# Optimization experiments

Hardware: AMD Instinct MI355X
Metric: run time of the kernel (lower is better)

The kernel has to match this reference:

```python
import jax, jax.numpy as jnp
import numpy as np

B, C, H, W = 2, 64, 128, 128
HEADS, DH = 8, 32
DN = ('NCHW', 'OIHW', 'NCHW')


def _conv(x, w, pad):
    return jax.lax.conv_general_dilated(x, w, (1, 1), [(pad, pad), (pad, pad)], dimension_numbers=DN)


def _rconv3(x, w):
    # Conv3x3 module: ReflectionPad2d(1) then 3x3 VALID conv, no bias
    xp = jnp.pad(x, ((0, 0), (0, 0), (1, 1), (1, 1)), mode='reflect')
    return jax.lax.conv_general_dilated(xp, w, (1, 1), 'VALID', dimension_numbers=DN)


def _prelu(x, a):
    return jnp.where(x > 0, x, a * x)


def _l2n(x):
    # F.normalize(p=2, dim=-1), eps=1e-12
    return x / jnp.maximum(jnp.linalg.norm(x, axis=-1, keepdims=True), 1e-12)


def _ln(y, g, b):
    mu = y.mean(-1, keepdims=True)
    v = ((y - mu) ** 2).mean(-1, keepdims=True)
    return (y - mu) / jnp.sqrt(v + 1e-5) * g + b


def _qco(x, w1, sw, sb, t1w, t1b, t2w, t2b):
    # QCO_C with level_num == C
    b, Cc = x.shape[0], x.shape[1]
    L = Cc
    x1 = _rconv3(x, w1)
    x_ave = _conv(jnp.mean(x1, (2, 3), keepdims=True), sw, 0) + sb[None, :, None, None]  # [b,C,1,1]
    xq = x_ave.reshape(b, Cc)
    mn = xq.min(-1, keepdims=True)
    mx = xq.max(-1, keepdims=True)
    qs = jnp.arange(L, dtype=x.dtype)
    ql = (2.0 * qs + 1.0) / (2.0 * L) * (mx - mn) + mn  # [b,L]
    inter = (ql[:, 1] - ql[:, 0])[:, None, None]  # [b,1,1]
    quant = 1.0 - jnp.abs(ql[:, None, :] - xq[:, :, None])  # [b,C,L]
    quant = quant * (quant > 1.0 - inter)
    sta = quant.sum(1)  # [b,L]
    sta = sta / sta.sum(-1, keepdims=True)
    out = jnp.concatenate([sta[:, :, None, None], x_ave], axis=1)  # [b,2C,1,1]
    out = jax.nn.relu(_conv(out, t1w, 0) + t1b[None, :, None, None])
    out = jax.nn.relu(_conv(out, t2w, 0) + t2b[None, :, None, None])
    return out  # [b,C,1,1]


def _attention(x, w_down, w_mid, w_up, wq_l, wk_m, wv_m, wq_h, rescale,
               w_proj_l, b_proj_l, w_proj_h, b_proj_h,
               qco_w1, qco_sca_w, qco_sca_b, qco_t1_w, qco_t1_b, qco_t2_w, qco_t2_b,
               rsp_w1, rsp_prelu, rsp_w2, c31_w1, c31_prelu, c31_w2, c31_w3):
    b, Cc, Hh, Ww = x.shape
    n = Hh * Ww
    # QKV conv projections (Conv2d, zero pad 1, no bias)
    xCL = jnp.moveaxis(_conv(x, w_down, 1), 1, -1)  # [b,h,w,C]
    xCM = jnp.moveaxis(_conv(x, w_mid, 1), 1, -1)   # [b,h,w,2C]
    xCH = jnp.moveaxis(_conv(x, w_up, 1), 1, -1)    # [b,h,w,3C]
    xL = xCL.reshape(b, n, Cc)
    xM = xCM.reshape(b, n, 2 * Cc)
    xH = xCH.reshape(b, n, 3 * Cc)

    def to_heads(t, d):  # [b,n,heads*d] -> [b,heads,d,n]
        return t.reshape(b, n, HEADS, d).transpose(0, 2, 3, 1)

    q_l = _l2n(to_heads(xL @ wq_l.T, DH))            # [b,heads,DH,n]
    k_m = _l2n(to_heads(xM @ wk_m.T, 2 * DH))        # [b,heads,2DH,n]
    v_m = to_heads(xM @ wv_m.T, 2 * DH)              # [b,heads,2DH,n]
    q_h = _l2n(to_heads(xH @ wq_h.T, 3 * DH))        # [b,heads,3DH,n]

    attn_l = jax.nn.softmax(jnp.einsum('bhdn,bhen->bhde', q_l, k_m) * rescale, axis=-1)  # [b,heads,DH,2DH]
    attn_h = jax.nn.softmax(jnp.einsum('bhdn,bhen->bhde', q_h, k_m) * rescale, axis=-1)  # [b,heads,3DH,2DH]

    x_l = jnp.einsum('bhde,bhen->bhdn', attn_l, v_m).transpose(0, 3, 1, 2).reshape(b, n, HEADS * DH)
    x_h = jnp.einsum('bhde,bhen->bhdn', attn_h, v_m).transpose(0, 3, 1, 2).reshape(b, n, HEADS * 3 * DH)
    # NOTE: torch code does .view(b, c, h, w) on [b, n, c] output -> raw memory reinterpretation,
    # which is exactly jnp.reshape here (faithful to the original, including this quirk).
    out_cl = (x_l @ w_proj_l.T + b_proj_l).reshape(b, Cc, Hh, Ww)
    out_ch = (x_h @ w_proj_h.T + b_proj_h).reshape(b, 3 * Cc, Hh, Ww)

    Hcat = jnp.concatenate([out_cl, out_ch], axis=1)  # [b,4C,h,w]
    H_out = _rconv3(_prelu(_rconv3(Hcat, rsp_w1), rsp_prelu), rsp_w2)  # ReshapeBlock -> [b,C,h,w]
    att_before = _qco(jnp.moveaxis(xCL, -1, 1), qco_w1, qco_sca_w, qco_sca_b,
                      qco_t1_w, qco_t1_b, qco_t2_w, qco_t2_b)  # [b,C,1,1]
    t = _prelu(_rconv3(H_out, c31_w1), c31_prelu)
    H_add = _conv(_rconv3(t, c31_w2), c31_w3, 0)  # Conv3_1
    return H_add + H_out * att_before


def _ff_block(z, g, bb, w1, b1, w2, b2):
    # PreNorm(LayerNorm over channel) + FeedForward(Linear, LeakyReLU(0.01), Linear)
    y = jnp.moveaxis(z, 1, -1)
    y = _ln(y, g, bb)
    y = y @ w1.T + b1
    y = jnp.where(y > 0, y, 0.01 * y)
    y = y @ w2.T + b2
    return jnp.moveaxis(y, -1, 1)


def _forward(x, w_down, w_mid, w_up, wq_l, wk_m, wv_m, wq_h, rescale,
             w_proj_l, b_proj_l, w_proj_h, b_proj_h,
             qco_w1, qco_sca_w, qco_sca_b, qco_t1_w, qco_t1_b, qco_t2_w, qco_t2_b,
             rsp_w1, rsp_prelu, rsp_w2, c31_w1, c31_prelu, c31_w2, c31_w3,
             ln1_g, ln1_b, ff1_w1, ff1_b1, ff1_w2, ff1_b2,
             ln2_g, ln2_b, ff2_w1, ff2_b1, ff2_w2, ff2_b2):
    out1 = _attention(x, w_down, w_mid, w_up, wq_l, wk_m, wv_m, wq_h, rescale,
                      w_proj_l, b_proj_l, w_proj_h, b_proj_h,
                      qco_w1, qco_sca_w, qco_sca_b, qco_t1_w, qco_t1_b, qco_t2_w, qco_t2_b,
                      rsp_w1, rsp_prelu, rsp_w2, c31_w1, c31_prelu, c31_w2, c31_w3) + x
    out2 = _ff_block(out1, ln1_g, ln1_b, ff1_w1, ff1_b1, ff1_w2, ff1_b2) + out1
    out3 = _ff_block(out2, ln2_g, ln2_b, ff2_w1, ff2_b1, ff2_w2, ff2_b2) + out1
    return out3


def setup_inputs() -> dict:
    keys = iter(jax.random.split(jax.random.key(0), 48))

    def rn(shape, s=0.05):
        return (jax.random.normal(next(keys), shape, jnp.float32) * s)

    d = {
        'x': rn((B, C, H, W), 1.0),
        'w_down': rn((C, C, 3, 3)), 'w_mid': rn((2 * C, C, 3, 3)), 'w_up': rn((3 * C, C, 3, 3)),
        'wq_l': rn((HEADS * DH, C)), 'wk_m': rn((2 * HEADS * DH, 2 * C)),
        'wv_m': rn((2 * HEADS * DH, 2 * C)), 'wq_h': rn((3 * HEADS * DH, 3 * C)),
        'rescale': jnp.ones((HEADS, 1, 1), jnp.float32),
        'w_proj_l': rn((C, HEADS * DH)), 'b_proj_l': rn((C,)),
        'w_proj_h': rn((3 * C, 3 * HEADS * DH)), 'b_proj_h': rn((3 * C,)),
        'qco_w1': rn((C, C, 3, 3)), 'qco_sca_w': rn((C, C, 1, 1)), 'qco_sca_b': rn((C,)),
        'qco_t1_w': rn((C, 2 * C, 1, 1)), 'qco_t1_b': rn((C,)),
        'qco_t2_w': rn((C, C, 1, 1)), 'qco_t2_b': rn((C,)),
        'rsp_w1': rn((C, 4 * C, 3, 3)), 'rsp_prelu': jnp.array(0.25, jnp.float32), 'rsp_w2': rn((C, C, 3, 3)),
        'c31_w1': rn((C, C, 3, 3)), 'c31_prelu': jnp.array(0.25, jnp.float32),
        'c31_w2': rn((C, C, 3, 3)), 'c31_w3': rn((C, C, 1, 1)),
        'ln1_g': jnp.ones((C,), jnp.float32), 'ln1_b': jnp.zeros((C,), jnp.float32),
        'ff1_w1': rn((C, C)), 'ff1_b1': rn((C,)), 'ff1_w2': rn((C, C)), 'ff1_b2': rn((C,)),
        'ln2_g': jnp.ones((C,), jnp.float32), 'ln2_b': jnp.zeros((C,), jnp.float32),
        'ff2_w1': rn((C, C)), 'ff2_b1': rn((C,)), 'ff2_w2': rn((C, C)), 'ff2_b2': rn((C,)),
    }
    return d


def reference(x, w_down, w_mid, w_up, wq_l, wk_m, wv_m, wq_h, rescale,
              w_proj_l, b_proj_l, w_proj_h, b_proj_h,
              qco_w1, qco_sca_w, qco_sca_b, qco_t1_w, qco_t1_b, qco_t2_w, qco_t2_b,
              rsp_w1, rsp_prelu, rsp_w2, c31_w1, c31_prelu, c31_w2, c31_w3,
              ln1_g, ln1_b, ff1_w1, ff1_b1, ff1_w2, ff1_b2,
              ln2_g, ln2_b, ff2_w1, ff2_b1, ff2_w2, ff2_b2):
    return _forward(x, w_down, w_mid, w_up, wq_l, wk_m, wv_m, wq_h, rescale,
                    w_proj_l, b_proj_l, w_proj_h, b_proj_h,
                    qco_w1, qco_sca_w, qco_sca_b, qco_t1_w, qco_t1_b, qco_t2_w, qco_t2_b,
                    rsp_w1, rsp_prelu, rsp_w2, c31_w1, c31_prelu, c31_w2, c31_w3,
                    ln1_g, ln1_b, ff1_w1, ff1_b1, ff1_w2, ff1_b2,
                    ln2_g, ln2_b, ff2_w1, ff2_b1, ff2_w2, ff2_b2)
```

## Files before the change

kernel.cpp:

```cpp
#include <hip/hip_runtime.h>
#include <hip/hip_bf16.h>
#include <stdint.h>

typedef __hip_bfloat16 bf16;
typedef __attribute__((ext_vector_type(8))) __bf16 bf8v;
typedef __attribute__((ext_vector_type(8))) short short8;
typedef __attribute__((ext_vector_type(4))) short short4v;
typedef __attribute__((ext_vector_type(4))) float f32x4;
#define DEVINL __device__ __forceinline__
#define MFMA16(a,b,c) __builtin_amdgcn_mfma_f32_16x16x32_bf16((a),(b),(c),0,0,0)

DEVINL short f2bs(float f) { bf16 h = __float2bfloat16(f); return *reinterpret_cast<short*>(&h); }
DEVINL float bs2f(short s) { bf16 h = *reinterpret_cast<bf16*>(&s); return __bfloat162float(h); }


static const size_t OFF_ZBF   = 0;
static const size_t OFF_WTQ   = 29360128;
static const size_t OFF_WTR1  = 29802496;
static const size_t OFF_WTR2  = 30097408;
static const size_t OFF_WTC1  = 30171136;
static const size_t OFF_WTF   = 30244864;
static const size_t OFF_W1T   = 30318592;
static const size_t OFF_SCAWT = 30466048;
static const size_t OFF_T1WT  = 30482432;
static const size_t OFF_T2WT  = 30515200;
static const size_t OFF_GB    = 31645696;
static const size_t OFF_WQLB  = 32235520;
static const size_t OFF_WKMB  = 32268288;
static const size_t OFF_WQHB  = 32399360;
static const size_t OFF_T1    = 41082880;
static const size_t OFF_UL    = 41345024;
static const size_t OFF_UK    = 41476096;
static const size_t OFF_T1H   = 42000384;
static const size_t OFF_UH    = 42786816;
static const size_t OFF_NORMS = 43966464;
static const size_t OFF_ATTL  = 43978752;
static const size_t OFF_ATTH  = 44109824;
static const size_t OFF_WEL   = 44503040;
static const size_t OFF_WEH   = 44765184;
static const size_t OFF_ACATB = 45813760;
static const size_t OFF_TSUM  = 45944832;
static const size_t OFF_ATTB  = 45949440;
static const size_t OFF_HCATB = 45949952;
static const size_t OFF_MIDB  = 62727168;
static const size_t OFF_HOUTB = 66921472;
static const size_t OFF_OUT1  = 71115776;
static const size_t OFF_GPART = 79504384;
static const size_t OFF_HCATT = 79504384;
static const size_t OFF_XT    = 98378752;
static const size_t WS_BYTES  = 102573056;

__global__ __launch_bounds__(256) void k_transp(const float* __restrict__ x,
                                                short* __restrict__ xt) {
  __shared__ short sT[64][72];
  const int t = threadIdx.x, b = blockIdx.z, p0 = blockIdx.x * 64;
  for (int i = t; i < 1024; i += 256) {
    int c = i >> 4, p4 = (i & 15) * 4;
    float4 g = *(const float4*)&x[(((size_t)(b * 64 + c)) << 14) + p0 + p4];
    sT[p4 + 0][c] = f2bs(g.x);
    sT[p4 + 1][c] = f2bs(g.y);
    sT[p4 + 2][c] = f2bs(g.z);
    sT[p4 + 3][c] = f2bs(g.w);
  }
  __syncthreads();
  for (int i = t; i < 512; i += 256) {
    int p = i >> 3, co = (i & 7) * 8;
    *(short8*)&xt[((((size_t)b << 14) + p0 + p)) * 64 + co] = *(short8*)&sT[p][co];
  }
}

__global__ __launch_bounds__(256) void k_transph(const short* __restrict__ hc,
                                                 short* __restrict__ ht) {
  __shared__ short sT[64][72];
  const int t = threadIdx.x, b = blockIdx.z, p0 = blockIdx.x * 64, c0 = blockIdx.y * 64;
  for (int i = t; i < 512; i += 256) {
    int c = i >> 3, qo = (i & 7) * 8;
    short8 v = *(const short8*)&hc[(((size_t)(b * 256 + c0 + c)) << 14) + p0 + qo];
#pragma unroll
    for (int u = 0; u < 8; u++) sT[qo + u][c] = v[u];
  }
  __syncthreads();
  for (int i = t; i < 512; i += 256) {
    int q = i >> 3, co = (i & 7) * 8;
    *(short8*)&ht[((size_t)(b * 16384 + p0 + q)) * 256 + c0 + co] = *(short8*)&sT[q][co];
  }
}

__global__ void k_prep_all(const float* __restrict__ wd, const float* __restrict__ wm,
                           const float* __restrict__ wu, const float* __restrict__ rw1,
                           const float* __restrict__ rw2, const float* __restrict__ cw1,
                           const float* __restrict__ wql, const float* __restrict__ wkm,
                           const float* __restrict__ wqh,
                           const float* __restrict__ c31w3, const float* __restrict__ c31w2,
                           const float* __restrict__ qw1, const float* __restrict__ qscaw,
                           const float* __restrict__ qt1w, const float* __restrict__ qt2w,
                           bf16* __restrict__ wtq, bf16* __restrict__ wtr1,
                           bf16* __restrict__ wtr2, bf16* __restrict__ wtc1,
                           bf16* __restrict__ wqlb, bf16* __restrict__ wkmb,
                           bf16* __restrict__ wqhb, bf16* __restrict__ wtf,
                           float* __restrict__ w1t, float* __restrict__ scawt,
                           float* __restrict__ t1wt, float* __restrict__ t2wt) {
  int i = blockIdx.x * 256 + threadIdx.x;
  if (i < 221184) {
    int tap = i / 24576, r = i % 24576, oc = r >> 6, ic = r & 63;
    float v;
    if (oc < 64)       v = wd[(oc * 64 + ic) * 9 + tap];
    else if (oc < 192) v = wm[((oc - 64) * 64 + ic) * 9 + tap];
    else               v = wu[((oc - 192) * 64 + ic) * 9 + tap];
    wtq[i] = __float2bfloat16(v);
  } else if (i < 368640) {
    int j = i - 221184;
    int tap = j / 16384, r = j % 16384, oc = r >> 8, ic = r & 255;
    wtr1[j] = __float2bfloat16(rw1[(oc * 256 + ic) * 9 + tap]);
  } else if (i < 405504) {
    int j = i - 368640;
    int tap = j / 4096, r = j % 4096, oc = r >> 6, ic = r & 63;
    wtr2[j] = __float2bfloat16(rw2[(oc * 64 + ic) * 9 + tap]);
  } else if (i < 442368) {
    int j = i - 405504;
    int tap = j / 4096, r = j % 4096, oc = r >> 6, ic = r & 63;
    wtc1[j] = __float2bfloat16(cw1[(oc * 64 + ic) * 9 + tap]);
  } else if (i < 458752) {
    int j = i - 442368; wqlb[j] = __float2bfloat16(wql[j]);
  } else if (i < 524288) {
    int j = i - 458752; wkmb[j] = __float2bfloat16(wkm[j]);
  } else if (i < 671744) {
    int j = i - 524288; wqhb[j] = __float2bfloat16(wqh[j]);
  } else if (i < 708608) {
    int j = i - 671744;
    int tap = j / 4096, r = j % 4096, o = r >> 6, ic = r & 63;
    float s = 0.f;
    for (int m = 0; m < 64; m++)
      s = fmaf(c31w3[o * 64 + m], c31w2[(m * 64 + ic) * 9 + tap], s);
    wtf[j] = __float2bfloat16(s);
  } else if (i < 745472) {
    int o = i - 708608;
    int c = o & 63, rest = o >> 6, jj = rest / 9, tap = rest % 9;
    w1t[o] = qw1[(c * 64 + jj) * 9 + tap];
  } else if (i < 749568) {
    int o = i - 745472;
    int c = o & 63, jj = o >> 6;
    scawt[o] = qscaw[c * 64 + jj];
  } else if (i < 757760) {
    int o = i - 749568;
    int c = o & 63, jj = o >> 6;
    t1wt[o] = qt1w[c * 128 + jj];
  } else if (i < 761856) {
    int o = i - 757760;
    int c = o & 63, jj = o >> 6;
    t2wt[o] = qt2w[c * 64 + jj];
  }
}

__global__ __launch_bounds__(256) void k_convq(
    const short* __restrict__ xt, const short* __restrict__ wtq,
    bf16* __restrict__ zbf)
{
  __shared__ short sX[3][130][72];
  const int t = threadIdx.x, lane = t & 63, wv = t >> 6;
  const int y = blockIdx.x, ocg = blockIdx.y, b = blockIdx.z;

  for (int i = t; i < 3120; i += 256) {
    int col = i % 130, rr = i / 130, row = rr % 3, ko = rr / 3;
    int gy = y + row - 1, gx = col - 1;
    short8 vv;
    if ((gy >= 0) & (gy < 128) & (gx >= 0) & (gx < 128)) {
      vv = *(const short8*)&xt[((size_t)b * 1048576 + (size_t)((gy << 7) + gx) * 64) + ko * 8];
    } else {
#pragma unroll
      for (int u = 0; u < 8; u++) vv[u] = 0;
    }
    *(short8*)&sX[row][col][ko * 8] = vv;
  }
  __syncthreads();

  const f32x4 zero = {0.f, 0.f, 0.f, 0.f};
  f32x4 acc[3][8];
#pragma unroll
  for (int m = 0; m < 3; m++)
#pragma unroll
    for (int n = 0; n < 8; n++) acc[m][n] = zero;

#pragma unroll
  for (int tap = 0; tap < 9; tap++) {
    const int ky = tap / 3, kx = tap % 3;
#pragma unroll
    for (int kk = 0; kk < 2; kk++) {
      const int kb = kk * 32 + (lane >> 4) * 8;
      bf8v a0 = *(const bf8v*)&wtq[(size_t)((tap * 384 + ocg * 192 + wv * 48 + (lane & 15)) * 64) + kb];
      bf8v a1 = *(const bf8v*)&wtq[(size_t)((tap * 384 + ocg * 192 + wv * 48 + 16 + (lane & 15)) * 64) + kb];
      bf8v a2 = *(const bf8v*)&wtq[(size_t)((tap * 384 + ocg * 192 + wv * 48 + 32 + (lane & 15)) * 64) + kb];
#pragma unroll
      for (int n = 0; n < 8; n++) {
        bf8v bfr = *(const bf8v*)&sX[ky][n * 16 + (lane & 15) + kx][kb];
        acc[0][n] = MFMA16(a0, bfr, acc[0][n]);
        acc[1][n] = MFMA16(a1, bfr, acc[1][n]);
        acc[2][n] = MFMA16(a2, bfr, acc[2][n]);
      }
    }
  }
#pragma unroll
  for (int m = 0; m < 3; m++) {
    const int oc0 = ocg * 192 + wv * 48 + m * 16 + ((lane >> 4) << 2);
#pragma unroll
    for (int n = 0; n < 8; n++) {
      const int px = n * 16 + (lane & 15);
#pragma unroll
      for (int r = 0; r < 4; r++)
        zbf[(((size_t)(b * 384 + oc0 + r)) << 14) + (y << 7) + px] = __float2bfloat16(acc[m][n][r]);
    }
  }
}

template<int EPI>
__global__ __launch_bounds__(256) void k_conv64(
    const short* __restrict__ in, int str, long bstride, int Cin,
    const short* __restrict__ Wt,
    short* __restrict__ outb, float* __restrict__ outf,
    const float* __restrict__ prelu_a,
    const short* __restrict__ houtpm, const float* __restrict__ attb,
    const float* __restrict__ x_nchw)
{
  __shared__ short sX[3][66][72];
  const int t = threadIdx.x, lane = t & 63, wv = t >> 6;
  const int y = blockIdx.x, x0 = blockIdx.y * 64, b = blockIdx.z;

  const f32x4 zero = {0.f, 0.f, 0.f, 0.f};
  f32x4 acc[4] = {zero, zero, zero, zero};

  for (int icb = 0; icb < Cin; icb += 64) {
    __syncthreads();
    for (int i = t; i < 1584; i += 256) {
      int col = i % 66, rr = i / 66, row = rr % 3, ko = rr / 3;
      int gy = y + row - 1, gx = x0 + col - 1;
      gy = gy < 0 ? 1 : (gy > 127 ? 126 : gy);
      gx = gx < 0 ? 1 : (gx > 127 ? 126 : gx);
      *(short8*)&sX[row][col][ko * 8] =
          *(const short8*)&in[(size_t)b * bstride + (size_t)((gy << 7) + gx) * str + icb + ko * 8];
    }
    __syncthreads();
#pragma unroll
    for (int tap = 0; tap < 9; tap++) {
      const int ky = tap / 3, kx = tap % 3;
#pragma unroll
      for (int kk = 0; kk < 2; kk++) {
        const int kb = kk * 32 + (lane >> 4) * 8;
        bf8v afr = *(const bf8v*)&Wt[(size_t)(tap * 64 + wv * 16 + (lane & 15)) * Cin + icb + kb];
#pragma unroll
        for (int n = 0; n < 4; n++) {
          bf8v bfr = *(const bf8v*)&sX[ky][n * 16 + (lane & 15) + kx][kb];
          acc[n] = MFMA16(afr, bfr, acc[n]);
        }
      }
    }
  }
  const int oc0 = wv * 16 + ((lane >> 4) << 2);
  const float aP = (EPI == 1) ? prelu_a[0] : 0.f;
#pragma unroll
  for (int n = 0; n < 4; n++) {
    const int gpx = (y << 7) + x0 + n * 16 + (lane & 15);
    if (EPI == 2) {
      short4v hv = *(const short4v*)&houtpm[((size_t)(b * 16384 + gpx)) * 64 + oc0];
      float4 av = *(const float4*)&attb[b * 64 + oc0];
      float4 o;
#pragma unroll
      for (int r = 0; r < 4; r++)
        (&o.x)[r] = acc[n][r] + bs2f(hv[r]) * (&av.x)[r] +
                    x_nchw[(((size_t)(b * 64 + oc0 + r)) << 14) + gpx];
      *(float4*)&outf[((size_t)(b * 16384 + gpx)) * 64 + oc0] = o;
    } else {
      short4v ss;
#pragma unroll
      for (int r = 0; r < 4; r++) {
        float v = acc[n][r];
        if (EPI == 1) v = v > 0.f ? v : aP * v;
        ss[r] = f2bs(v);
      }
      *(short4v*)&outb[((size_t)(b * 16384 + gpx)) * 64 + oc0] = ss;
    }
  }
}

__global__ __launch_bounds__(256) void k_gramm(const short* __restrict__ Z,
                                               float* __restrict__ Gp) {
  int rem = blockIdx.x, ti = 0;
  while (rem >= 6 - ti) { rem -= 6 - ti; ti++; }
  const int tj = ti + rem;
  const int kc = blockIdx.y, b = blockIdx.z;
  __shared__ short sA[64][72];
  __shared__ short sB[64][72];
  const int t = threadIdx.x, lane = t & 63, wv = t >> 6;
  const int wo = wv & 1, wp = wv >> 1;
  const f32x4 zero = {0.f, 0.f, 0.f, 0.f};
  f32x4 acc[2][2];
#pragma unroll
  for (int m = 0; m < 2; m++)
#pragma unroll
    for (int n = 0; n < 2; n++) acc[m][n] = zero;
  const size_t zb = (size_t)b * 6291456;
  const int k0 = kc * 1024;
  for (int ks = 0; ks < 1024; ks += 64) {
    __syncthreads();
    for (int i = t; i < 512; i += 256) {
      int r = i >> 3, ko = i & 7;
      *(short8*)&sA[r][ko * 8] =
          *(const short8*)&Z[zb + ((size_t)(ti * 64 + r) << 14) + k0 + ks + ko * 8];
      *(short8*)&sB[r][ko * 8] =
          *(const short8*)&Z[zb + ((size_t)(tj * 64 + r) << 14) + k0 + ks + ko * 8];
    }
    __syncthreads();
#pragma unroll
    for (int kk = 0; kk < 2; kk++) {
      const int kb = kk * 32 + (lane >> 4) * 8;
// ... 135 lines not shown
};

__global__ __launch_bounds__(256) void k_sgemm2b(Jobs2 J, bf16* __restrict__ Cb) {
  __shared__ float sa[16][17];
  __shared__ float sb[16][17];
  const int bx = blockIdx.x, z = blockIdx.y;
  int j = (bx >= J.b0[1]) ? 1 : 0;
  const int local = bx - J.b0[j];
  const int x = local % J.nx[j], y = local / J.nx[j];
  const int tx = threadIdx.x & 15, ty = threadIdx.x >> 4;
  const float* Ap = J.A[j];
  const float* Bp = J.B[j] + (size_t)z * J.sB[j];
  const int K = J.K[j], lda = J.lda[j];
  const int m = y * 16 + ty, n = x * 16 + tx;
  float acc = 0.f;
  for (int k0 = 0; k0 < K; k0 += 16) {
    sa[ty][tx] = Ap[(size_t)m * lda + k0 + tx];
    sb[ty][tx] = Bp[(size_t)(k0 + ty) * 128 + n];
    __syncthreads();
#pragma unroll
    for (int kk = 0; kk < 16; kk++) acc = fmaf(sa[ty][kk], sb[kk][tx], acc);
    __syncthreads();
  }
  Cb[(size_t)z * 32768 + J.co[j] + (size_t)m * 128 + n] = __float2bfloat16(acc);
}

__global__ __launch_bounds__(256) void k_norms2(
    const float* __restrict__ UL, const float* __restrict__ UK,
    const float* __restrict__ UH,
    const float* __restrict__ wql, const float* __restrict__ wkm,
    const float* __restrict__ wqh, float* __restrict__ norms) {
  const int t = threadIdx.x, lane = t & 63;
  const int row = blockIdx.x * 4 + (t >> 6);
  const int b = row >> 11 ? 1 : (row >= 1536 ? 1 : 0);
  const int r = row - b * 1536;
  const float* u; const float* wv; int K;
  if (r < 256)      { K = 64;  u = UL + (size_t)(b * 256 + r) * 64;          wv = wql + (size_t)r * 64; }
  else if (r < 768) { int e = r - 256; K = 128; u = UK + (size_t)(b * 512 + e) * 128; wv = wkm + (size_t)e * 128; }
  else              { int d = r - 768; K = 192; u = UH + (size_t)(b * 768 + d) * 192; wv = wqh + (size_t)d * 192; }
  float s = 0.f;
  for (int k = lane; k < K; k += 64) s = fmaf(u[k], wv[k], s);
#pragma unroll
  for (int o = 32; o; o >>= 1) s += __shfl_xor(s, o);
  if (lane == 0) norms[b * 1536 + r] = fmaxf(sqrtf(fmaxf(s, 0.f)), 1e-12f);
}

__global__ __launch_bounds__(256) void k_attn(
    const float* __restrict__ T1, const float* __restrict__ T1H,
    const float* __restrict__ wkm, const float* __restrict__ norms,
    const float* __restrict__ rescale,
    float* __restrict__ attL, float* __restrict__ attH)
{
  const int h = blockIdx.x, cy = blockIdx.y, b = blockIdx.z;
  const int t = threadIdx.x;
  __shared__ float sK[64 * 129];
  __shared__ float sQ[32 * 129];
  __shared__ float sNk[64];
  const int isL = (cy == 0);
  const int rbase = isL ? 0 : (cy - 1) * 32;
  const float* TQ = isL ? (T1 + (size_t)(b * 256 + h * 32) * 128)
                        : (T1H + (size_t)(b * 768 + h * 96 + rbase) * 128);
  for (int idx = t; idx < 8192; idx += 256) {
    int e = idx >> 7, k = idx & 127;
    sK[e * 129 + k] = wkm[(size_t)(h * 64 + e) * 128 + k];
  }
  for (int idx = t; idx < 4096; idx += 256) {
    int r = idx >> 7, k = idx & 127;
// ... 132 lines not shown
  sm[c] = acc * (1.f / 16384.f);
  __syncthreads();
  float xa = scab[c];
  for (int j = 0; j < 64; j++) xa = fmaf(scawt[(j << 6) + c], sm[j], xa);
  sxq[c] = xa;
  __syncthreads();
  float mn = xa, mx = xa;
#pragma unroll
  for (int o = 32; o; o >>= 1) {
    mn = fminf(mn, __shfl_xor(mn, o));
    mx = fmaxf(mx, __shfl_xor(mx, o));
  }
  float inter = (mx - mn) * (1.f / 64.f);
  float ql = (2.f * c + 1.f) / 128.f * (mx - mn) + mn;
  float sta = 0.f;
  for (int j = 0; j < 64; j++) {
    float q = 1.f - fabsf(ql - sxq[j]);
    sta += (q > 1.f - inter) ? q : 0.f;
  }
  float tot = sta;
#pragma unroll
  for (int o = 32; o; o >>= 1) tot += __shfl_xor(tot, o);
  sta = sta / fmaxf(tot, 1e-30f);
  scat[c] = sta; scat[64 + c] = xa;
  __syncthreads();
  float h = t1b[c];
  for (int j = 0; j < 128; j++) h = fmaf(t1wt[(j << 6) + c], scat[j], h);
  h = fmaxf(h, 0.f);
  sh1[c] = h;
  __syncthreads();
  float o2 = t2b[c];
  for (int j = 0; j < 64; j++) o2 = fmaf(t2wt[(j << 6) + c], sh1[j], o2);
  attb[b * 64 + c] = fmaxf(o2, 0.f);
}

__global__ __launch_bounds__(256) void k_ffm2(const float* __restrict__ out1pm,
    const float* g1, const float* be1, const float* w11, const float* b11,
    const float* w12, const float* b12,
    const float* g2, const float* be2, const float* w21, const float* b21,
    const float* w22, const float* b22,
    float* __restrict__ outp)
{
  __shared__ short sW4[4][64][72];
  __shared__ short sy[128][72];
  __shared__ float spar[8][64];

  const int t = threadIdx.x, lane = t & 63, wv = t >> 6;
  const int gp0 = blockIdx.x * 128;
  const int b = gp0 >> 14, p0 = gp0 & 16383;
  const int chq = ((lane >> 4) << 2);

  for (int idx = t; idx < 4096; idx += 256) {
    int oc = idx >> 6, k = idx & 63;
    sW4[0][oc][k] = f2bs(w11[idx]);
    sW4[1][oc][k] = f2bs(w12[idx]);
    sW4[2][oc][k] = f2bs(w21[idx]);
    sW4[3][oc][k] = f2bs(w22[idx]);
  }
  if (t < 64) {
    spar[0][t] = g1[t]; spar[1][t] = be1[t]; spar[2][t] = b11[t]; spar[3][t] = b12[t];
    spar[4][t] = g2[t]; spar[5][t] = be2[t]; spar[6][t] = b21[t]; spar[7][t] = b22[t];
  }
  float4 vv[4][2];
#pragma unroll
  for (int m = 0; m < 4; m++)
#pragma unroll
    for (int n = 0; n < 2; n++) {
      const int px = p0 + wv * 32 + n * 16 + (lane & 15);
      vv[m][n] = *(const float4*)&out1pm[((size_t)(b * 16384 + px)) * 64 + m * 16 + chq];
    }
  __syncthreads();

  const f32x4 zero = {0.f, 0.f, 0.f, 0.f};
  f32x4 acc[4][2];

#define LN_REG(SRCV, GI, BI)                                                     \
  {                                                                              \
    _Pragma("unroll")                                                            \
    for (int n = 0; n < 2; n++) {                                                \
      float s1 = 0.f, s2 = 0.f;                                                  \
      _Pragma("unroll")                                                          \
      for (int m = 0; m < 4; m++)                                                \
        _Pragma("unroll")                                                        \
        for (int r = 0; r < 4; r++) {                                            \
          float vx = (&SRCV[m][n].x)[r];                                         \
          s1 += vx; s2 += vx * vx;                                               \
        }                                                                        \
      s1 += __shfl_xor(s1, 16); s1 += __shfl_xor(s1, 32);                        \
      s2 += __shfl_xor(s2, 16); s2 += __shfl_xor(s2, 32);                        \
      float mu = s1 * (1.f / 64.f);                                              \
      float var = fmaxf(s2 * (1.f / 64.f) - mu * mu, 0.f);                       \
      float rstd = 1.f / sqrtf(var + 1e-5f);                                     \
      const int pxl = wv * 32 + n * 16 + (lane & 15);                            \
      _Pragma("unroll")                                                          \
      for (int m = 0; m < 4; m++) {                                              \
        short4v ss;                                                              \
        _Pragma("unroll")                                                        \
        for (int r = 0; r < 4; r++) {                                            \
          int ch = m * 16 + chq + r;                                             \
          ss[r] = f2bs(((&SRCV[m][n].x)[r] - mu) * rstd * spar[GI][ch] + spar[BI][ch]); \
        }                                                                        \
        *(short4v*)&sy[pxl][m * 16 + chq] = ss;                                  \
      }                                                                          \
    }                                                                            \
  }

#define MM_STAGE(SIDX)                                                           \
  {                                                                              \
    _Pragma("unroll")                                                            \
    for (int m = 0; m < 4; m++) { acc[m][0] = zero; acc[m][1] = zero; }          \
    _Pragma("unroll")                                                            \
    for (int kk = 0; kk < 2; kk++) {                                             \
      const int kb = kk * 32 + (lane >> 4) * 8;                                  \
      bf8v bfr0 = *(const bf8v*)&sy[wv * 32 + (lane & 15)][kb];                  \
      bf8v bfr1 = *(const bf8v*)&sy[wv * 32 + 16 + (lane & 15)][kb];             \
      _Pragma("unroll")                                                          \
      for (int m = 0; m < 4; m++) {                                              \
        bf8v afr = *(const bf8v*)&sW4[SIDX][m * 16 + (lane & 15)][kb];           \
        acc[m][0] = MFMA16(afr, bfr0, acc[m][0]);                                \
        acc[m][1] = MFMA16(afr, bfr1, acc[m][1]);                                \
      }                                                                          \
    }                                                                            \
  }

  LN_REG(vv, 0, 1);
  __syncthreads();
  MM_STAGE(0);
#pragma unroll
  for (int m = 0; m < 4; m++) {
#pragma unroll
    for (int n = 0; n < 2; n++) {
      const int pxl = wv * 32 + n * 16 + (lane & 15);
      short4v ss;
#pragma unroll
      for (int r = 0; r < 4; r++) {
        float h = acc[m][n][r] + spar[2][m * 16 + chq + r];
        h = h > 0.f ? h : 0.01f * h;
        ss[r] = f2bs(h);
      }
      *(short4v*)&sy[pxl][m * 16 + chq] = ss;
    }
  }
  __syncthreads();
  MM_STAGE(1);
  float4 o2v[4][2];
#pragma unroll
  for (int m = 0; m < 4; m++)
#pragma unroll
    for (int n = 0; n < 2; n++)
#pragma unroll
      for (int r = 0; r < 4; r++)
        (&o2v[m][n].x)[r] = acc[m][n][r] + spar[3][m * 16 + chq + r] + (&vv[m][n].x)[r];
  LN_REG(o2v, 4, 5);
  __syncthreads();
  MM_STAGE(2);
#pragma unroll
  for (int m = 0; m < 4; m++) {
#pragma unroll
    for (int n = 0; n < 2; n++) {
      const int pxl = wv * 32 + n * 16 + (lane & 15);
      short4v ss;
#pragma unroll
      for (int r = 0; r < 4; r++) {
        float h = acc[m][n][r] + spar[6][m * 16 + chq + r];
        h = h > 0.f ? h : 0.01f * h;
        ss[r] = f2bs(h);
      }
      *(short4v*)&sy[pxl][m * 16 + chq] = ss;
    }
  }
  __syncthreads();
  MM_STAGE(3);
#pragma unroll
  for (int m = 0; m < 4; m++)
#pragma unroll
    for (int n = 0; n < 2; n++) {
      const int pxl = wv * 32 + n * 16 + (lane & 15);
#pragma unroll
      for (int r = 0; r < 4; r++) {
        const int ch = m * 16 + chq + r;
        outp[(((size_t)(b * 64 + ch)) << 14) + p0 + pxl] =
            acc[m][n][r] + spar[7][ch] + (&vv[m][n].x)[r];
      }
    }
#undef LN_REG
#undef MM_STAGE
}

extern "C" void kernel_launch(void* const* d_in, const int* in_sizes, int n_in,
                              void* d_out, int out_size, void* d_ws, size_t ws_size,
                              hipStream_t stream)
{
  if (ws_size < WS_BYTES) return;
  char* ws = (char*)d_ws;

  const float* x       = (const float*)d_in[0];
  const float* w_down  = (const float*)d_in[1];
  const float* w_mid   = (const float*)d_in[2];
  const float* w_up    = (const float*)d_in[3];
  const float* wq_l    = (const float*)d_in[4];
  const float* wk_m    = (const float*)d_in[5];
  const float* wv_m    = (const float*)d_in[6];
  const float* wq_h    = (const float*)d_in[7];
  const float* rescale = (const float*)d_in[8];
  const float* w_proj_l= (const float*)d_in[9];
  const float* b_proj_l= (const float*)d_in[10];
  const float* w_proj_h= (const float*)d_in[11];
  const float* b_proj_h= (const float*)d_in[12];
  const float* qco_w1  = (const float*)d_in[13];
  const float* qsca_w  = (const float*)d_in[14];
  const float* qsca_b  = (const float*)d_in[15];
  const float* qt1_w   = (const float*)d_in[16];
  const float* qt1_b   = (const float*)d_in[17];
  const float* qt2_w   = (const float*)d_in[18];
  const float* qt2_b   = (const float*)d_in[19];
  const float* rsp_w1  = (const float*)d_in[20];
  const float* rsp_pr  = (const float*)d_in[21];
  const float* rsp_w2  = (const float*)d_in[22];
  const float* c31_w1  = (const float*)d_in[23];
// ... 15 lines not shown

  bf16*  zbf   = (bf16*)(ws + OFF_ZBF);
  bf16*  wtq   = (bf16*)(ws + OFF_WTQ);
  bf16*  wtr1  = (bf16*)(ws + OFF_WTR1);
  bf16*  wtr2  = (bf16*)(ws + OFF_WTR2);
  bf16*  wtc1  = (bf16*)(ws + OFF_WTC1);
  bf16*  wtf   = (bf16*)(ws + OFF_WTF);
  float* w1t   = (float*)(ws + OFF_W1T);
  float* scawt = (float*)(ws + OFF_SCAWT);
  float* t1wt  = (float*)(ws + OFF_T1WT);
  float* t2wt  = (float*)(ws + OFF_T2WT);
  bf16*  Gb    = (bf16*)(ws + OFF_GB);
  bf16*  wqlb  = (bf16*)(ws + OFF_WQLB);
  bf16*  wkmb  = (bf16*)(ws + OFF_WKMB);
  bf16*  wqhb  = (bf16*)(ws + OFF_WQHB);
  float* gpart = (float*)(ws + OFF_GPART);
  float* T1    = (float*)(ws + OFF_T1);
  float* UL    = (float*)(ws + OFF_UL);
  float* UK    = (float*)(ws + OFF_UK);
  float* T1H   = (float*)(ws + OFF_T1H);
  float* UH    = (float*)(ws + OFF_UH);
  float* norms = (float*)(ws + OFF_NORMS);
  float* attL  = (float*)(ws + OFF_ATTL);
  float* attH  = (float*)(ws + OFF_ATTH);
  float* WeL   = (float*)(ws + OFF_WEL);
  float* WeH   = (float*)(ws + OFF_WEH);
  bf16*  acatb = (bf16*)(ws + OFF_ACATB);
  float* tsum  = (float*)(ws + OFF_TSUM);
  float* attb  = (float*)(ws + OFF_ATTB);
  bf16*  hcatb = (bf16*)(ws + OFF_HCATB);
  short* hcatT = (short*)(ws + OFF_HCATT);
  short* midb  = (short*)(ws + OFF_MIDB);
  short* houtb = (short*)(ws + OFF_HOUTB);
  float* out1  = (float*)(ws + OFF_OUT1);
  short* xt    = (short*)(ws + OFF_XT);

  k_transp<<<dim3(256, 1, 2), 256, 0, stream>>>(x, xt);
  k_prep_all<<<dim3(2976), 256, 0, stream>>>(
      w_down, w_mid, w_up, rsp_w1, rsp_w2, c31_w1, wq_l, wk_m, wq_h,
      c31_w3, c31_w2, qco_w1, qsca_w, qt1_w, qt2_w,
      wtq, wtr1, wtr2, wtc1, wqlb, wkmb, wqhb, wtf,
      w1t, scawt, t1wt, t2wt);

  k_convq<<<dim3(128, 2, 2), 256, 0, stream>>>(xt, (const short*)wtq, zbf);

  k_gramm<<<dim3(21, 16, 2), 256, 0, stream>>>((const short*)zbf, gpart);
  k_gredb<<<dim3(1152), 256, 0, stream>>>(gpart, Gb);

  k_tsum2<<<dim3(128), 256, 0, stream>>>(zbf, tsum);

  MJobs5 M5;
  M5.A[0] = (const short*)wqlb; M5.lda[0] = 64;  M5.K[0] = 64;  M5.r0[0] = 0;   M5.c0[0] = 64;  M5.C[0] = T1;  M5.ldc[0] = 128; M5.sC[0] = 32768;  M5.nx[0] = 2;
  M5.A[1] = (const short*)wqlb; M5.lda[1] = 64;  M5.K[1] = 64;  M5.r0[1] = 0;   M5.c0[1] = 0;   M5.C[1] = UL;  M5.ldc[1] = 64;  M5.sC[1] = 16384;  M5.nx[1] = 1;
  M5.A[2] = (const short*)wkmb; M5.lda[2] = 128; M5.K[2] = 128; M5.r0[2] = 64;  M5.c0[2] = 64;  M5.C[2] = UK;  M5.ldc[2] = 128; M5.sC[2] = 65536;  M5.nx[2] = 2;
  M5.A[3] = (const short*)wqhb; M5.lda[3] = 192; M5.K[3] = 192; M5.r0[3] = 192; M5.c0[3] = 64;  M5.C[3] = T1H; M5.ldc[3] = 128; M5.sC[3] = 98304;  M5.nx[3] = 2;
  M5.A[4] = (const short*)wqhb; M5.lda[4] = 192; M5.K[4] = 192; M5.r0[4] = 192; M5.c0[4] = 192; M5.C[4] = UH;  M5.ldc[4] = 192; M5.sC[4] = 147456; M5.nx[4] = 3;
  M5.b0[0] = 0; M5.b0[1] = 8; M5.b0[2] = 12; M5.b0[3] = 28; M5.b0[4] = 52; M5.b0[5] = 88;
  k_mgemm5<<<dim3(88, 2), 256, 0, stream>>>(M5, (const short*)Gb);

  k_norms2<<<dim3(768), 256, 0, stream>>>(UL, UK, UH, wq_l, wk_m, wq_h, norms);
  k_qco<<<dim3(2), 64, 0, stream>>>(tsum, w1t, scawt, qsca_b, t1wt, qt1_b, t2wt, qt2_b, attb);
  k_attn<<<dim3(8, 4, 2), 256, 0, stream>>>(T1, T1H, wk_m, norms, rescale, attL, attH);
  k_weff<<<dim3(8, 2, 2), 256, 0, stream>>>(attL, attH, wv_m, WeL, WeH);

  Jobs2 J2;
  J2.A[0] = w_proj_l; J2.B[0] = WeL; J2.K[0] = 256; J2.lda[0] = 256; J2.sB[0] = 32768; J2.nx[0] = 8; J2.co[0] = 0;
  J2.A[1] = w_proj_h; J2.B[1] = WeH; J2.K[1] = 768; J2.lda[1] = 768; J2.sB[1] = 98304; J2.nx[1] = 8; J2.co[1] = 8192;
  J2.b0[0] = 0; J2.b0[1] = 32; J2.b0[2] = 128;
  k_sgemm2b<<<dim3(128, 2), 256, 0, stream>>>(J2, acatb);

  k_pixm<<<dim3(256, 4, 2), 256, 0, stream>>>((const short*)zbf, (const short*)acatb,
                                              b_proj_l, b_proj_h, hcatb);

  k_transph<<<dim3(256, 4, 2), 256, 0, stream>>>((const short*)hcatb, hcatT);

  k_conv64<1><<<dim3(128, 2, 2), 256, 0, stream>>>(
      hcatT, 256, 4194304L, 256,
      (const short*)wtr1, midb, nullptr, rsp_pr, nullptr, nullptr, nullptr);
  k_conv64<0><<<dim3(128, 2, 2), 256, 0, stream>>>(
      midb, 64, 1048576L, 64,
      (const short*)wtr2, houtb, nullptr, nullptr, nullptr, nullptr, nullptr);

  k_conv64<1><<<dim3(128, 2, 2), 256, 0, stream>>>(
      houtb, 64, 1048576L, 64,
      (const short*)wtc1, midb, nullptr, c31_pr, nullptr, nullptr, nullptr);
  k_conv64<2><<<dim3(128, 2, 2), 256, 0, stream>>>(
      midb, 64, 1048576L, 64,
      (const short*)wtf, nullptr, out1, nullptr, houtb, attb, x);

  k_ffm2<<<dim3(256), 256, 0, stream>>>(out1,
      ln1_g, ln1_b, ff1_w1, ff1_b1, ff1_w2, ff1_b2,
      ln2_g, ln2_b, ff2_w1, ff2_b1, ff2_w2, ff2_b2,
      (float*)d_out);
}
```

Measured before the change: 282.9 us.

## Fuse final 3x3 conv with LayerNorm and feedforward stages into one kernel

The final fused 3x3 conv (with residual and attention-scale epilogue) now runs in the same kernel as the two LayerNorm+MLP feedforward stages. The fp32 intermediate out1 is no longer written to and re-read from global memory. The FF weights are converted to bf16 once in the prep kernel instead of in every ffm block. The staging-load index order in the conv kernels is also swapped so consecutive threads read consecutive 16-byte chunks. In exchange, each conv block carries more LDS and registers, and each wave reads FF weights from global memory rather than LDS.

```diff
diff --git a/kernel.cpp b/kernel.cpp
--- a/kernel.cpp
+++ b/kernel.cpp
@@ -44,7 +44,7 @@
 static const size_t OFF_HCATB = 45949952;
 static const size_t OFF_MIDB  = 62727168;
 static const size_t OFF_HOUTB = 66921472;
-static const size_t OFF_OUT1  = 71115776;
+static const size_t OFF_WFFB  = 71115776;
 static const size_t OFF_GPART = 79504384;
 static const size_t OFF_HCATT = 79504384;
 static const size_t OFF_XT    = 98378752;
@@ -94,12 +94,15 @@
                            const float* __restrict__ c31w3, const float* __restrict__ c31w2,
                            const float* __restrict__ qw1, const float* __restrict__ qscaw,
                            const float* __restrict__ qt1w, const float* __restrict__ qt2w,
+                           const float* __restrict__ f11, const float* __restrict__ f12,
+                           const float* __restrict__ f21, const float* __restrict__ f22,
                            bf16* __restrict__ wtq, bf16* __restrict__ wtr1,
                            bf16* __restrict__ wtr2, bf16* __restrict__ wtc1,
                            bf16* __restrict__ wqlb, bf16* __restrict__ wkmb,
                            bf16* __restrict__ wqhb, bf16* __restrict__ wtf,
                            float* __restrict__ w1t, float* __restrict__ scawt,
-                           float* __restrict__ t1wt, float* __restrict__ t2wt) {
+                           float* __restrict__ t1wt, float* __restrict__ t2wt,
+                           bf16* __restrict__ wffb) {
   int i = blockIdx.x * 256 + threadIdx.x;
   if (i < 221184) {
     int tap = i / 24576, r = i % 24576, oc = r >> 6, ic = r & 63;
@@ -149,6 +152,11 @@
     int o = i - 757760;
     int c = o & 63, jj = o >> 6;
     t2wt[o] = qt2w[c * 64 + jj];
+  } else if (i < 778240) {
+    int j = i - 761856;
+    int stage = j >> 12, r = j & 4095;
+    const float* src = (stage == 0) ? f11 : (stage == 1) ? f12 : (stage == 2) ? f21 : f22;
+    wffb[j] = __float2bfloat16(src[r]);
   }
 }
 
@@ -161,7 +169,7 @@
   const int y = blockIdx.x, ocg = blockIdx.y, b = blockIdx.z;
 
   for (int i = t; i < 3120; i += 256) {
-    int col = i % 130, rr = i / 130, row = rr % 3, ko = rr / 3;
+    int ko = i & 7, c2 = i >> 3, col = c2 % 130, row = c2 / 130;
     int gy = y + row - 1, gx = col - 1;
     short8 vv;
     if ((gy >= 0) & (gy < 128) & (gx >= 0) & (gx < 128)) {
@@ -216,10 +224,8 @@
 __global__ __launch_bounds__(256) void k_conv64(
     const short* __restrict__ in, int str, long bstride, int Cin,
     const short* __restrict__ Wt,
-    short* __restrict__ outb, float* __restrict__ outf,
-    const float* __restrict__ prelu_a,
-    const short* __restrict__ houtpm, const float* __restrict__ attb,
-    const float* __restrict__ x_nchw)
+    short* __restrict__ outb,
+    const float* __restrict__ prelu_a)
 {
   __shared__ short sX[3][66][72];
   const int t = threadIdx.x, lane = t & 63, wv = t >> 6;
@@ -231,7 +237,7 @@
   for (int icb = 0; icb < Cin; icb += 64) {
     __syncthreads();
     for (int i = t; i < 1584; i += 256) {
-      int col = i % 66, rr = i / 66, row = rr % 3, ko = rr / 3;
+      int ko = i & 7, c2 = i >> 3, col = c2 % 66, row = c2 / 66;
       int gy = y + row - 1, gx = x0 + col - 1;
       gy = gy < 0 ? 1 : (gy > 127 ? 126 : gy);
       gx = gx < 0 ? 1 : (gx > 127 ? 126 : gx);
@@ -259,26 +265,180 @@
 #pragma unroll
   for (int n = 0; n < 4; n++) {
     const int gpx = (y << 7) + x0 + n * 16 + (lane & 15);
-    if (EPI == 2) {
+    short4v ss;
+#pragma unroll
+    for (int r = 0; r < 4; r++) {
+      float v = acc[n][r];
+      if (EPI == 1) v = v > 0.f ? v : aP * v;
+      ss[r] = f2bs(v);
+    }
+    *(short4v*)&outb[((size_t)(b * 16384 + gpx)) * 64 + oc0] = ss;
+  }
+}
+
+__global__ __launch_bounds__(256) void k_convff(
+    const short* __restrict__ in,
+    const short* __restrict__ Wt,
+    const short* __restrict__ houtpm,
+    const float* __restrict__ attb,
+    const float* __restrict__ x_nchw,
+    const short* __restrict__ wffb,
+    const float* __restrict__ g1, const float* __restrict__ be1,
+    const float* __restrict__ b11, const float* __restrict__ b12,
+    const float* __restrict__ g2, const float* __restrict__ be2,
+    const float* __restrict__ b21, const float* __restrict__ b22,
+    float* __restrict__ outp)
+{
+  __shared__ short sX[3][66][72];
+  __shared__ float sv[64][68];
+  __shared__ short sy[64][72];
+  __shared__ float spar[8][64];
+  const int t = threadIdx.x, lane = t & 63, wv = t >> 6;
+  const int y = blockIdx.x, x0 = blockIdx.y * 64, b = blockIdx.z;
+
+  if (t < 64) {
+    spar[0][t] = g1[t]; spar[1][t] = be1[t]; spar[2][t] = b11[t]; spar[3][t] = b12[t];
+    spar[4][t] = g2[t]; spar[5][t] = be2[t]; spar[6][t] = b21[t]; spar[7][t] = b22[t];
+  }
+  for (int i = t; i < 1584; i += 256) {
+    int ko = i & 7, c2 = i >> 3, col = c2 % 66, row = c2 / 66;
+    int gy = y + row - 1, gx = x0 + col - 1;
+    gy = gy < 0 ? 1 : (gy > 127 ? 126 : gy);
+    gx = gx < 0 ? 1 : (gx > 127 ? 126 : gx);
+    *(short8*)&sX[row][col][ko * 8] =
+        *(const short8*)&in[(size_t)b * 1048576 + (size_t)((gy << 7) + gx) * 64 + ko * 8];
+  }
+  __syncthreads();
+
+  const f32x4 zero = {0.f, 0.f, 0.f, 0.f};
+  {
+    f32x4 cacc[4] = {zero, zero, zero, zero};
+#pragma unroll
+    for (int tap = 0; tap < 9; tap++) {
+      const int ky = tap / 3, kx = tap % 3;
+#pragma unroll
+      for (int kk = 0; kk < 2; kk++) {
+        const int kb = kk * 32 + (lane >> 4) * 8;
+        bf8v afr = *(const bf8v*)&Wt[(size_t)(tap * 64 + wv * 16 + (lane & 15)) * 64 + kb];
+#pragma unroll
+        for (int n = 0; n < 4; n++) {
+          bf8v bfr = *(const bf8v*)&sX[ky][n * 16 + (lane & 15) + kx][kb];
+          cacc[n] = MFMA16(afr, bfr, cacc[n]);
+        }
+      }
+    }
+    const int oc0 = wv * 16 + ((lane >> 4) << 2);
+    float4 av = *(const float4*)&attb[b * 64 + oc0];
+#pragma unroll
+    for (int n = 0; n < 4; n++) {
+      const int pxl = n * 16 + (lane & 15);
+      const int gpx = (y << 7) + x0 + pxl;
       short4v hv = *(const short4v*)&houtpm[((size_t)(b * 16384 + gpx)) * 64 + oc0];
-      float4 av = *(const float4*)&attb[b * 64 + oc0];
-      float4 o;
 #pragma unroll
       for (int r = 0; r < 4; r++)
-        (&o.x)[r] = acc[n][r] + bs2f(hv[r]) * (&av.x)[r] +
-                    x_nchw[(((size_t)(b * 64 + oc0 + r)) << 14) + gpx];
-      *(float4*)&outf[((size_t)(b * 16384 + gpx)) * 64 + oc0] = o;
-    } else {
-      short4v ss;
-#pragma unroll
-      for (int r = 0; r < 4; r++) {
-        float v = acc[n][r];
-        if (EPI == 1) v = v > 0.f ? v : aP * v;
-        ss[r] = f2bs(v);
-      }
-      *(short4v*)&outb[((size_t)(b * 16384 + gpx)) * 64 + oc0] = ss;
-    }
-  }
+        sv[pxl][oc0 + r] = cacc[n][r] + bs2f(hv[r]) * (&av.x)[r] +
+                           x_nchw[(((size_t)(b * 64 + oc0 + r)) << 14) + gpx];
+    }
+  }
+  __syncthreads();
+
+  const int chq = ((lane >> 4) << 2);
+  const int pxl = wv * 16 + (lane & 15);
+  float4 vv[4];
+#pragma unroll
+  for (int m = 0; m < 4; m++) vv[m] = *(const float4*)&sv[pxl][m * 16 + chq];
+
+  f32x4 facc[4];
+
+#define LN_F(SRCV, GI, BI)                                                      \
+  {                                                                             \
+    float s1 = 0.f, s2 = 0.f;                                                   \
+    _Pragma("unroll")                                                           \
+    for (int m = 0; m < 4; m++)                                                 \
+      _Pragma("unroll")                                                         \
+      for (int r = 0; r < 4; r++) {                                             \
+        float vx = (&SRCV[m].x)[r];                                             \
+        s1 += vx; s2 += vx * vx;                                                \
+      }                                                                         \
+    s1 += __shfl_xor(s1, 16); s1 += __shfl_xor(s1, 32);                         \
+    s2 += __shfl_xor(s2, 16); s2 += __shfl_xor(s2, 32);                         \
+    float mu = s1 * (1.f / 64.f);                                               \
+    float var = fmaxf(s2 * (1.f / 64.f) - mu * mu, 0.f);                        \
+    float rstd = 1.f / sqrtf(var + 1e-5f);                                      \
+    _Pragma("unroll")                                                           \
+    for (int m = 0; m < 4; m++) {                                               \
+      short4v ss;                                                               \
+      _Pragma("unroll")                                                         \
+      for (int r = 0; r < 4; r++) {                                             \
+        int ch = m * 16 + chq + r;                                              \
+        ss[r] = f2bs(((&SRCV[m].x)[r] - mu) * rstd * spar[GI][ch] + spar[BI][ch]); \
+      }                                                                         \
+      *(short4v*)&sy[pxl][m * 16 + chq] = ss;                                   \
+    }                                                                           \
+  }
+
+#define MM_F(SIDX)                                                              \
+  {                                                                             \
+    _Pragma("unroll")                                                           \
+    for (int m = 0; m < 4; m++) facc[m] = zero;                                 \
+    _Pragma("unroll")                                                           \
+    for (int kk = 0; kk < 2; kk++) {                                            \
+      const int kb = kk * 32 + (lane >> 4) * 8;                                 \
+      bf8v bfr = *(const bf8v*)&sy[wv * 16 + (lane & 15)][kb];                  \
+      _Pragma("unroll")                                                         \
+      for (int m = 0; m < 4; m++) {                                             \
+        bf8v afr = *(const bf8v*)&wffb[(size_t)(SIDX) * 4096 +                  \
+                                       (m * 16 + (lane & 15)) * 64 + kb];       \
+        facc[m] = MFMA16(afr, bfr, facc[m]);                                    \
+      }                                                                         \
+    }                                                                           \
+  }
+
+  LN_F(vv, 0, 1);
+  MM_F(0);
+#pragma unroll
+  for (int m = 0; m < 4; m++) {
+    short4v ss;
+#pragma unroll
+    for (int r = 0; r < 4; r++) {
+      float h = facc[m][r] + spar[2][m * 16 + chq + r];
+      h = h > 0.f ? h : 0.01f * h;
+      ss[r] = f2bs(h);
+    }
+    *(short4v*)&sy[pxl][m * 16 + chq] = ss;
+  }
+  MM_F(1);
+  float4 o2v[4];
+#pragma unroll
+  for (int m = 0; m < 4; m++)
+#pragma unroll
+    for (int r = 0; r < 4; r++)
+      (&o2v[m].x)[r] = facc[m][r] + spar[3][m * 16 + chq + r] + (&vv[m].x)[r];
+  LN_F(o2v, 4, 5);
+  MM_F(2);
+#pragma unroll
+  for (int m = 0; m < 4; m++) {
+    short4v ss;
+#pragma unroll
+    for (int r = 0; r < 4; r++) {
+      float h = facc[m][r] + spar[6][m * 16 + chq + r];
+      h = h > 0.f ? h : 0.01f * h;
+      ss[r] = f2bs(h);
+    }
+    *(short4v*)&sy[pxl][m * 16 + chq] = ss;
+  }
+  MM_F(3);
+  const int gpx = (y << 7) + x0 + pxl;
+#pragma unroll
+  for (int m = 0; m < 4; m++)
+#pragma unroll
+    for (int r = 0; r < 4; r++) {
+      const int ch = m * 16 + chq + r;
+      outp[(((size_t)(b * 64 + ch)) << 14) + gpx] =
+          facc[m][r] + spar[7][ch] + (&vv[m].x)[r];
+    }
+#undef LN_F
+#undef MM_F
 }
 
 __global__ __launch_bounds__(256) void k_gramm(const short* __restrict__ Z,
@@ -480,7 +640,7 @@
     const float* __restrict__ wqh, float* __restrict__ norms) {
   const int t = threadIdx.x, lane = t & 63;
   const int row = blockIdx.x * 4 + (t >> 6);
-  const int b = row >> 11 ? 1 : (row >= 1536 ? 1 : 0);
+  const int b = row >= 1536 ? 1 : 0;
   const int r = row - b * 1536;
   const float* u; const float* wv; int K;
   if (r < 256)      { K = 64;  u = UL + (size_t)(b * 256 + r) * 64;          wv = wql + (size_t)r * 64; }
@@ -679,159 +839,6 @@
   float o2 = t2b[c];
   for (int j = 0; j < 64; j++) o2 = fmaf(t2wt[(j << 6) + c], sh1[j], o2);
   attb[b * 64 + c] = fmaxf(o2, 0.f);
-}
-
-__global__ __launch_bounds__(256) void k_ffm2(const float* __restrict__ out1pm,
-    const float* g1, const float* be1, const float* w11, const float* b11,
-    const float* w12, const float* b12,
-    const float* g2, const float* be2, const float* w21, const float* b21,
-    const float* w22, const float* b22,
-    float* __restrict__ outp)
-{
-  __shared__ short sW4[4][64][72];
-  __shared__ short sy[128][72];
-  __shared__ float spar[8][64];
-
-  const int t = threadIdx.x, lane = t & 63, wv = t >> 6;
-  const int gp0 = blockIdx.x * 128;
-  const int b = gp0 >> 14, p0 = gp0 & 16383;
-  const int chq = ((lane >> 4) << 2);
-
-  for (int idx = t; idx < 4096; idx += 256) {
-    int oc = idx >> 6, k = idx & 63;
-    sW4[0][oc][k] = f2bs(w11[idx]);
-    sW4[1][oc][k] = f2bs(w12[idx]);
-    sW4[2][oc][k] = f2bs(w21[idx]);
-    sW4[3][oc][k] = f2bs(w22[idx]);
-  }
-  if (t < 64) {
-    spar[0][t] = g1[t]; spar[1][t] = be1[t]; spar[2][t] = b11[t]; spar[3][t] = b12[t];
-    spar[4][t] = g2[t]; spar[5][t] = be2[t]; spar[6][t] = b21[t]; spar[7][t] = b22[t];
-  }
-  float4 vv[4][2];
-#pragma unroll
-  for (int m = 0; m < 4; m++)
-#pragma unroll
-    for (int n = 0; n < 2; n++) {
-      const int px = p0 + wv * 32 + n * 16 + (lane & 15);
-      vv[m][n] = *(const float4*)&out1pm[((size_t)(b * 16384 + px)) * 64 + m * 16 + chq];
-    }
-  __syncthreads();
-
-  const f32x4 zero = {0.f, 0.f, 0.f, 0.f};
-  f32x4 acc[4][2];
-
-#define LN_REG(SRCV, GI, BI)                                                     \
-  {                                                                              \
-    _Pragma("unroll")                                                            \
-    for (int n = 0; n < 2; n++) {                                                \
-      float s1 = 0.f, s2 = 0.f;                                                  \
-      _Pragma("unroll")                                                          \
-      for (int m = 0; m < 4; m++)                                                \
-        _Pragma("unroll")                                                        \
-        for (int r = 0; r < 4; r++) {                                            \
-          float vx = (&SRCV[m][n].x)[r];                                         \
-          s1 += vx; s2 += vx * vx;                                               \
-        }                                                                        \
-      s1 += __shfl_xor(s1, 16); s1 += __shfl_xor(s1, 32);                        \
-      s2 += __shfl_xor(s2, 16); s2 += __shfl_xor(s2, 32);                        \
-      float mu = s1 * (1.f / 64.f);                                              \
-      float var = fmaxf(s2 * (1.f / 64.f) - mu * mu, 0.f);                       \
-      float rstd = 1.f / sqrtf(var + 1e-5f);                                     \
-      const int pxl = wv * 32 + n * 16 + (lane & 15);                            \
-      _Pragma("unroll")                                                          \
-      for (int m = 0; m < 4; m++) {                                              \
-        short4v ss;                                                              \
-        _Pragma("unroll")                                                        \
-        for (int r = 0; r < 4; r++) {                                            \
-          int ch = m * 16 + chq + r;                                             \
-          ss[r] = f2bs(((&SRCV[m][n].x)[r] - mu) * rstd * spar[GI][ch] + spar[BI][ch]); \
-        }                                                                        \
-        *(short4v*)&sy[pxl][m * 16 + chq] = ss;                                  \
-      }                                                                          \
-    }                                                                            \
-  }
-
-#define MM_STAGE(SIDX)                                                           \
-  {                                                                              \
-    _Pragma("unroll")                                                            \
-    for (int m = 0; m < 4; m++) { acc[m][0] = zero; acc[m][1] = zero; }          \
-    _Pragma("unroll")                                                            \
-    for (int kk = 0; kk < 2; kk++) {                                             \
-      const int kb = kk * 32 + (lane >> 4) * 8;                                  \
-      bf8v bfr0 = *(const bf8v*)&sy[wv * 32 + (lane & 15)][kb];                  \
-      bf8v bfr1 = *(const bf8v*)&sy[wv * 32 + 16 + (lane & 15)][kb];             \
-      _Pragma("unroll")                                                          \
-      for (int m = 0; m < 4; m++) {                                              \
-        bf8v afr = *(const bf8v*)&sW4[SIDX][m * 16 + (lane & 15)][kb];           \
-        acc[m][0] = MFMA16(afr, bfr0, acc[m][0]);                                \
-        acc[m][1] = MFMA16(afr, bfr1, acc[m][1]);                                \
-      }                                                                          \
-    }                                                                            \
-  }
-
-  LN_REG(vv, 0, 1);
-  __syncthreads();
-  MM_STAGE(0);
-#pragma unroll
-  for (int m = 0; m < 4; m++) {
-#pragma unroll
-    for (int n = 0; n < 2; n++) {
-      const int pxl = wv * 32 + n * 16 + (lane & 15);
-      short4v ss;
-#pragma unroll
-      for (int r = 0; r < 4; r++) {
-        float h = acc[m][n][r] + spar[2][m * 16 + chq + r];
-        h = h > 0.f ? h : 0.01f * h;
-        ss[r] = f2bs(h);
-      }
-      *(short4v*)&sy[pxl][m * 16 + chq] = ss;
-    }
-  }
-  __syncthreads();
-  MM_STAGE(1);
-  float4 o2v[4][2];
-#pragma unroll
-  for (int m = 0; m < 4; m++)
-#pragma unroll
-    for (int n = 0; n < 2; n++)
-#pragma unroll
-      for (int r = 0; r < 4; r++)
-        (&o2v[m][n].x)[r] = acc[m][n][r] + spar[3][m * 16 + chq + r] + (&vv[m][n].x)[r];
-  LN_REG(o2v, 4, 5);
-  __syncthreads();
-  MM_STAGE(2);
-#pragma unroll
-  for (int m = 0; m < 4; m++) {
-#pragma unroll
-    for (int n = 0; n < 2; n++) {
-      const int pxl = wv * 32 + n * 16 + (lane & 15);
-      short4v ss;
-#pragma unroll
-      for (int r = 0; r < 4; r++) {
-        float h = acc[m][n][r] + spar[6][m * 16 + chq + r];
-        h = h > 0.f ? h : 0.01f * h;
-        ss[r] = f2bs(h);
-      }
-      *(short4v*)&sy[pxl][m * 16 + chq] = ss;
-    }
-  }
-  __syncthreads();
-  MM_STAGE(3);
-#pragma unroll
-  for (int m = 0; m < 4; m++)
-#pragma unroll
-    for (int n = 0; n < 2; n++) {
-      const int pxl = wv * 32 + n * 16 + (lane & 15);
-#pragma unroll
-      for (int r = 0; r < 4; r++) {
-        const int ch = m * 16 + chq + r;
-        outp[(((size_t)(b * 64 + ch)) << 14) + p0 + pxl] =
-            acc[m][n][r] + spar[7][ch] + (&vv[m][n].x)[r];
-      }
-    }
-#undef LN_REG
-#undef MM_STAGE
 }
 
 extern "C" void kernel_launch(void* const* d_in, const int* in_sizes, int n_in,
@@ -913,15 +920,16 @@
   short* hcatT = (short*)(ws + OFF_HCATT);
   short* midb  = (short*)(ws + OFF_MIDB);
   short* houtb = (short*)(ws + OFF_HOUTB);
-  float* out1  = (float*)(ws + OFF_OUT1);
+  bf16*  wffb  = (bf16*)(ws + OFF_WFFB);
   short* xt    = (short*)(ws + OFF_XT);
 
   k_transp<<<dim3(256, 1, 2), 256, 0, stream>>>(x, xt);
-  k_prep_all<<<dim3(2976), 256, 0, stream>>>(
+  k_prep_all<<<dim3(3040), 256, 0, stream>>>(
       w_down, w_mid, w_up, rsp_w1, rsp_w2, c31_w1, wq_l, wk_m, wq_h,
       c31_w3, c31_w2, qco_w1, qsca_w, qt1_w, qt2_w,
+      ff1_w1, ff1_w2, ff2_w1, ff2_w2,
       wtq, wtr1, wtr2, wtc1, wqlb, wkmb, wqhb, wtf,
-      w1t, scawt, t1wt, t2wt);
+      w1t, scawt, t1wt, t2wt, wffb);
 
   k_convq<<<dim3(128, 2, 2), 256, 0, stream>>>(xt, (const short*)wtq, zbf);
 
@@ -956,21 +964,15 @@
   k_transph<<<dim3(256, 4, 2), 256, 0, stream>>>((const short*)hcatb, hcatT);
 
   k_conv64<1><<<dim3(128, 2, 2), 256, 0, stream>>>(
-      hcatT, 256, 4194304L, 256,
-      (const short*)wtr1, midb, nullptr, rsp_pr, nullptr, nullptr, nullptr);
+      hcatT, 256, 4194304L, 256, (const short*)wtr1, midb, rsp_pr);
   k_conv64<0><<<dim3(128, 2, 2), 256, 0, stream>>>(
-      midb, 64, 1048576L, 64,
-      (const short*)wtr2, houtb, nullptr, nullptr, nullptr, nullptr, nullptr);
+      midb, 64, 1048576L, 64, (const short*)wtr2, houtb, nullptr);
 
   k_conv64<1><<<dim3(128, 2, 2), 256, 0, stream>>>(
-      houtb, 64, 1048576L, 64,
-      (const short*)wtc1, midb, nullptr, c31_pr, nullptr, nullptr, nullptr);
-  k_conv64<2><<<dim3(128, 2, 2), 256, 0, stream>>>(
-      midb, 64, 1048576L, 64,
-      (const short*)wtf, nullptr, out1, nullptr, houtb, attb, x);
-
-  k_ffm2<<<dim3(256), 256, 0, stream>>>(out1,
-      ln1_g, ln1_b, ff1_w1, ff1_b1, ff1_w2, ff1_b2,
-      ln2_g, ln2_b, ff2_w1, ff2_b1, ff2_w2, ff2_b2,
+      houtb, 64, 1048576L, 64, (const short*)wtc1, midb, c31_pr);
+
+  k_convff<<<dim3(128, 2, 2), 256, 0, stream>>>(
+      midb, (const short*)wtf, houtb, attb, x, (const short*)wffb,
+      ln1_g, ln1_b, ff1_b1, ff1_b2, ln2_g, ln2_b, ff2_b1, ff2_b2,
       (float*)d_out);
 }
```

Result: faster. 271.5 us (-4.0%).
